# Performance work log

Measured on AMD Instinct MI355X. Metric: run time of the kernel, lower is better.

Reference implementation:

```python
import jax, jax.numpy as jnp
import numpy as np

GROUPS = 32
EPS = 1e-5
NUM_HEADS = 8


def group_norm(x, gamma, beta):
    B, C, H, W = x.shape
    xg = x.reshape(B, GROUPS, C // GROUPS, H, W)
    mean = xg.mean(axis=(2, 3, 4), keepdims=True)
    var = xg.var(axis=(2, 3, 4), keepdims=True)
    xg = (xg - mean) * jax.lax.rsqrt(var + EPS)
    x = xg.reshape(B, C, H, W)
    return x * gamma[None, :, None, None] + beta[None, :, None, None]


def setup_inputs() -> dict:
    key = jax.random.key(0)
    k1, k2, k3 = jax.random.split(key, 3)
    C = 512
    x = jax.random.normal(k1, (16, C, 32, 32), dtype=jnp.float32)
    gn_gamma = jnp.ones((C,), dtype=jnp.float32)
    gn_beta = jnp.zeros((C,), dtype=jnp.float32)
    w_qkv = jax.random.normal(k2, (3 * C, C), dtype=jnp.float32) * 0.02
    b_qkv = jnp.zeros((3 * C,), dtype=jnp.float32)
    w_proj = jax.random.normal(k3, (C, C), dtype=jnp.float32) * 0.02
    b_proj = jnp.zeros((C,), dtype=jnp.float32)
    return {"x": x, "gn_gamma": gn_gamma, "gn_beta": gn_beta,
            "w_qkv": w_qkv, "b_qkv": b_qkv, "w_proj": w_proj, "b_proj": b_proj}


def reference(x, gn_gamma, gn_beta, w_qkv, b_qkv, w_proj, b_proj):
    B, C, H, W = x.shape
    nh = NUM_HEADS
    hd = C // nh
    h = group_norm(x, gn_gamma, gn_beta)
    # 1x1 conv == channel matmul: [B,3C,H,W]
    qkv = jnp.einsum('bchw,oc->bohw', h, w_qkv) + b_qkv[None, :, None, None]
    qkv = qkv.reshape(B, 3, nh, hd, H * W)
    q, k, v = qkv[:, 0], qkv[:, 1], qkv[:, 2]  # [B, nh, hd, HW]
    scale = hd ** -0.5
    # attn[b,n,i,j] = sum_d q[b,n,d,i] * k[b,n,d,j]
    attn = jax.nn.softmax(jnp.einsum('bndi,bndj->bnij', q, k) * scale, axis=-1)
    # h[b,n,d,i] = sum_j v[b,n,d,j] * attn[b,n,i,j]
    h = jnp.einsum('bndj,bnij->bndi', v, attn).reshape(B, C, H, W)
    out = jnp.einsum('bchw,oc->bohw', h, w_proj) + b_proj[None, :, None, None]
    return x + out
```

## Files before the change

### kernel.cpp

```cpp
#include <hip/hip_runtime.h>

typedef __bf16 bf16;
typedef __bf16 bf16x2 __attribute__((ext_vector_type(2)));
typedef __bf16 bf16x4 __attribute__((ext_vector_type(4)));
typedef __bf16 bf16x8 __attribute__((ext_vector_type(8)));
typedef float  f32x4  __attribute__((ext_vector_type(4)));
typedef float  f32x16 __attribute__((ext_vector_type(16)));
typedef unsigned int u32x4 __attribute__((ext_vector_type(4)));

#define MFMA32(a,b,c) __builtin_amdgcn_mfma_f32_32x32x16_bf16((a),(b),(c),0,0,0)

#if __has_builtin(__builtin_amdgcn_exp2f)
#define EXP2(x) __builtin_amdgcn_exp2f(x)
#else
#define EXP2(x) exp2f(x)
#endif

__device__ __forceinline__ void gll16(const void* g, void* l) {
  __builtin_amdgcn_global_load_lds((const __attribute__((address_space(1))) unsigned int*)g,
                                   (__attribute__((address_space(3))) unsigned int*)l, 16, 0, 0);
}

__device__ __forceinline__ unsigned pk2(float a, float b) {
  bf16x2 t = { (bf16)a, (bf16)b };
  return __builtin_bit_cast(unsigned, t);
}

__device__ __forceinline__ void pl32swap(unsigned &x, unsigned &y) {
  asm("v_permlane32_swap_b32 %0, %1" : "+v"(x), "+v"(y));
}

static constexpr int Cc = 512;
static constexpr int Ss = 1024;
#define QSCALE 0.18033688011112042f

__global__ __launch_bounds__(256) void k_wconv(const float* __restrict__ wq, const float* __restrict__ wp,
                                               bf16* __restrict__ wqb, bf16* __restrict__ wpb) {
  const int i = blockIdx.x * 256 + threadIdx.x;
  if (i * 4 < 786432) {
    float4 v = ((const float4*)wq)[i];
    bf16x4 o = { (bf16)v.x, (bf16)v.y, (bf16)v.z, (bf16)v.w };
    ((bf16x4*)wqb)[i] = o;
  } else {
    const int j = i - 786432 / 4;
    float4 v = ((const float4*)wp)[j];
    bf16x4 o = { (bf16)v.x, (bf16)v.y, (bf16)v.z, (bf16)v.w };
    ((bf16x4*)wpb)[j] = o;
  }
}

__global__ __launch_bounds__(256, 2) void k_gnorm(const float* __restrict__ x,
                                                  const float* __restrict__ gamma,
                                                  const float* __restrict__ beta,
                                                  bf16* __restrict__ ht) {
  const int g = blockIdx.x;
  const int b = blockIdx.y;
  const float* base = x + ((size_t)b * Cc + g * 16) * Ss;
  const int tid = threadIdx.x;

  f32x4 xr[16];
  float s = 0.f, sq = 0.f;
  #pragma unroll
  for (int k = 0; k < 16; ++k) {
    xr[k] = ((const f32x4*)base)[k * 256 + tid];
    s  += xr[k][0] + xr[k][1] + xr[k][2] + xr[k][3];
    sq += xr[k][0] * xr[k][0] + xr[k][1] * xr[k][1] + xr[k][2] * xr[k][2] + xr[k][3] * xr[k][3];
  }
  #pragma unroll
  for (int m = 1; m < 64; m <<= 1) { s += __shfl_xor(s, m); sq += __shfl_xor(sq, m); }
  __shared__ float red[8];
  if ((tid & 63) == 0) { red[tid >> 6] = s; red[4 + (tid >> 6)] = sq; }
  __syncthreads();
  const float stot = red[0] + red[1] + red[2] + red[3];
  const float sqt  = red[4] + red[5] + red[6] + red[7];
  const float mean = stot * (1.f / 16384.f);
  const float var  = sqt * (1.f / 16384.f) - mean * mean;
  const float rstd = rsqrtf(var + 1e-5f);

  float ga[16], bb[16];
  #pragma unroll
  for (int k = 0; k < 16; ++k) {
    ga[k] = gamma[g * 16 + k] * rstd;
    bb[k] = beta[g * 16 + k] - mean * ga[k];
  }

  bf16* dst0 = ht + ((size_t)b * Ss + tid * 4) * Cc + g * 16;
  #pragma unroll
  for (int j = 0; j < 4; ++j) {
    bf16x8 o0, o1;
    #pragma unroll
    for (int k = 0; k < 8; ++k)  o0[k] = (bf16)(xr[k][j] * ga[k] + bb[k]);
    #pragma unroll
    for (int k = 0; k < 8; ++k)  o1[k] = (bf16)(xr[8 + k][j] * ga[8 + k] + bb[8 + k]);
    bf16* d = dst0 + (size_t)j * Cc;
    *(bf16x8*)d = o0;
    *(bf16x8*)(d + 8) = o1;
  }
}

template<int MODE>
__global__ __launch_bounds__(256, 2) void k_gemm(const bf16* __restrict__ Aw,
                                                 const bf16* __restrict__ Bt,
                                                 const float* __restrict__ bias,
                                                 bf16* __restrict__ qo, bf16* __restrict__ ko,
                                                 bf16* __restrict__ vo,
                                                 const float* __restrict__ xres,
                                                 float* __restrict__ out) {
  const int nt = blockIdx.x, mt = blockIdx.y, b = blockIdx.z;
  const int M0 = mt * 128, N0 = nt * 128;
  __shared__ __align__(16) char lA[2][16384];
  __shared__ __align__(16) char lB[2][16384];
  const int tid = threadIdx.x;
  const int l = tid & 63, w = tid >> 6;
  const int wm = w >> 1, wn = w & 1;
  const int l31 = l & 31, h = l >> 5;
  const bf16* Bb = Bt + (size_t)b * Ss * Cc;

  const int r8 = tid >> 3, c8 = tid & 7;
  const int csw = (c8 ^ (r8 & 7)) * 16;
  const char* asrc = (const char*)Aw + (size_t)(M0 + r8) * 1024 + csw;
  const char* bsrc = (const char*)Bb + (size_t)(N0 + r8) * 1024 + csw;
  const int dstoff = tid * 16;

  f32x16 acc[2][2];
  #pragma unroll
  for (int i = 0; i < 2; ++i)
    #pragma unroll
    for (int j = 0; j < 2; ++j)
      #pragma unroll
      for (int r = 0; r < 16; ++r) acc[i][j][r] = 0.f;

  const int sw7 = l31 & 7;

  #pragma unroll
  for (int p = 0; p < 4; ++p)
    gll16(asrc + (size_t)p * 32768, (char*)lA[0] + dstoff + p * 4096);
  #pragma unroll
  for (int p = 0; p < 4; ++p)
    gll16(bsrc + (size_t)p * 32768, (char*)lB[0] + dstoff + p * 4096);

  #pragma unroll
  for (int kt = 0; kt < 8; ++kt) {
    const int cur = kt & 1;
    if (kt < 7) {
      #pragma unroll
      for (int p = 0; p < 4; ++p)
        gll16(asrc + (size_t)p * 32768 + (kt + 1) * 128, (char*)lA[cur ^ 1] + dstoff + p * 4096);
      #pragma unroll
      for (int p = 0; p < 4; ++p)
        gll16(bsrc + (size_t)p * 32768 + (kt + 1) * 128, (char*)lB[cur ^ 1] + dstoff + p * 4096);
      asm volatile("s_waitcnt vmcnt(8)" ::: "memory");
    } else {
      asm volatile("s_waitcnt vmcnt(0)" ::: "memory");
    }
    __builtin_amdgcn_s_barrier();
    __builtin_amdgcn_sched_barrier(0);

    __builtin_amdgcn_s_setprio(1);
    #pragma unroll
    for (int kb = 0; kb < 4; ++kb) {
      const int cA0 = ((kb * 2 + h) ^ sw7) * 16;
      const int rA0 = (wm * 2 + 0) * 32 + l31, rA1 = (wm * 2 + 1) * 32 + l31;
      const int rB0 = (wn * 2 + 0) * 32 + l31, rB1 = (wn * 2 + 1) * 32 + l31;
      bf16x8 a0 = *(const bf16x8*)((const char*)lA[cur] + rA0 * 128 + cA0);
      bf16x8 a1 = *(const bf16x8*)((const char*)lA[cur] + rA1 * 128 + cA0);
      bf16x8 b0 = *(const bf16x8*)((const char*)lB[cur] + rB0 * 128 + cA0);
      bf16x8 b1 = *(const bf16x8*)((const char*)lB[cur] + rB1 * 128 + cA0);
      acc[0][0] = MFMA32(a0, b0, acc[0][0]);
      acc[0][1] = MFMA32(a0, b1, acc[0][1]);
      acc[1][0] = MFMA32(a1, b0, acc[1][0]);
      acc[1][1] = MFMA32(a1, b1, acc[1][1]);
    }
    __builtin_amdgcn_s_setprio(0);
    if (kt < 7) {
      asm volatile("s_waitcnt lgkmcnt(0)" ::: "memory");
      __builtin_amdgcn_s_barrier();
    }
  }

  #pragma unroll
  for (int m = 0; m < 2; ++m) {
    const int ofr = M0 + wm * 64 + m * 32;
    #pragma unroll
    for (int n = 0; n < 2; ++n) {
      const int sI = N0 + wn * 64 + n * 32 + l31;
      #pragma unroll
      for (int Qi = 0; Qi < 4; ++Qi) {
        const int rb = Qi * 8 + h * 4;
        float v[4], bi[4];
        #pragma unroll
        for (int r = 0; r < 4; ++r) {
          v[r] = acc[m][n][Qi * 4 + r];
          bi[r] = bias[ofr + rb + r];
        }
        if (MODE == 0) {
          const int which = ofr >> 9;
          const int nh = (ofr >> 6) & 7;
          const int dbase = (ofr & 63) + rb;
          const size_t bh = (size_t)b * 8 + nh;
          if (which == 2) {
            #pragma unroll
            for (int r = 0; r < 4; ++r)
              vo[(bh * 64 + dbase + r) * 1024 + sI] = (bf16)(v[r] + bi[r]);
          } else {
            const float qs = which ? 1.f : QSCALE;
            bf16x4 pk = { (bf16)((v[0] + bi[0]) * qs), (bf16)((v[1] + bi[1]) * qs),
                          (bf16)((v[2] + bi[2]) * qs), (bf16)((v[3] + bi[3]) * qs) };
            bf16* dst = (which ? ko : qo) + (bh * 1024 + sI) * 64 + dbase;
            *(bf16x4*)dst = pk;
          }
        } else {
          #pragma unroll
          for (int r = 0; r < 4; ++r) {
            const size_t idx = ((size_t)b * 512 + ofr + rb + r) * 1024 + sI;
            out[idx] = xres[idx] + bi[r] + v[r];
          }
        }
      }
    }
  }
}

__global__ __launch_bounds__(512, 3) void k_attn(const bf16* __restrict__ qT,
                                                 const bf16* __restrict__ kT,
                                                 const bf16* __restrict__ vv,
                                                 bf16* __restrict__ ao) {
  const int it = blockIdx.x, nh = blockIdx.y, b = blockIdx.z;
  const size_t bh = (size_t)b * 8 + nh;
  const char* kh = (const char*)(kT + bh * 65536);
  const char* vh = (const char*)(vv + bh * 65536);
  __shared__ __align__(16) char smem[32768];
  const int tid = threadIdx.x;
  const int w = tid >> 6, l = tid & 63;
  const int l31 = l & 31, h = l >> 5;

  const int ct = tid >> 6, c3 = ct & 3, c2 = ct >> 2;
  const char* ksrc = kh + (size_t)(c2 * 32 + l31) * 128 + c3 * 32 + h * 16;
  const char* vsrc = vh + (size_t)(c2 * 32 + l31) * 2048 + c3 * 32 + h * 16;
  char* lkdst = smem + tid * 16;
  char* lvdst = smem + 16384 + tid * 16;

  gll16(ksrc, lkdst);
  gll16(vsrc, lvdst);

  const bf16* qrow = qT + bh * 65536 + (size_t)(it * 256 + w * 32 + l31) * 64;
  bf16x8 qf[4];
  #pragma unroll
  for (int kq = 0; kq < 4; ++kq) qf[kq] = *(const bf16x8*)(qrow + kq * 16 + h * 8);

  f32x16 oacc[2];
  #pragma unroll
  for (int dt = 0; dt < 2; ++dt)
    #pragma unroll
    for (int r = 0; r < 16; ++r) oacc[dt][r] = 0.f;
  float lacc0 = 0.f, lacc1 = 0.f;

  int cur = 0;
  for (int t = 0; t < 16; ++t) {
    if (t < 15) {
      gll16(ksrc + (size_t)(t + 1) * 8192, lkdst + (cur ^ 1) * 8192);
      gll16(vsrc + (size_t)(t + 1) * 128,  lvdst + (cur ^ 1) * 8192);
      asm volatile("s_waitcnt vmcnt(2)" ::: "memory");
    } else {
      asm volatile("s_waitcnt vmcnt(0)" ::: "memory");
    }
    __builtin_amdgcn_s_barrier();
    __builtin_amdgcn_sched_barrier(0);

    const char* lkc = smem + cur * 8192;
    const char* lvc = smem + 16384 + cur * 8192;

    f32x16 sf[2];
    #pragma unroll
    for (int r = 0; r < 16; ++r) { sf[0][r] = 0.f; sf[1][r] = 0.f; }
    __builtin_amdgcn_s_setprio(1);
    #pragma unroll
    for (int kq = 0; kq < 4; ++kq) {
      bf16x8 a0 = *(const bf16x8*)(lkc + kq * 1024 + l * 16);
      bf16x8 a1 = *(const bf16x8*)(lkc + (4 + kq) * 1024 + l * 16);
      sf[0] = MFMA32(a0, qf[kq], sf[0]);
      sf[1] = MFMA32(a1, qf[kq], sf[1]);
    }
    __builtin_amdgcn_s_setprio(0);

    unsigned pw[2][4][2];
    #pragma unroll
    for (int jt = 0; jt < 2; ++jt) {
      #pragma unroll
      for (int Qi = 0; Qi < 4; ++Qi) {
        const float p0 = EXP2(sf[jt][Qi * 4 + 0]);
        const float p1 = EXP2(sf[jt][Qi * 4 + 1]);
        const float p2 = EXP2(sf[jt][Qi * 4 + 2]);
        const float p3 = EXP2(sf[jt][Qi * 4 + 3]);
        lacc0 += p0 + p1; lacc1 += p2 + p3;
        pw[jt][Qi][0] = pk2(p0, p1);
        pw[jt][Qi][1] = pk2(p2, p3);
      }
    }

    bf16x8 pb[4];
    #pragma unroll
    for (int s = 0; s < 4; ++s) {
      const int jt = s >> 1, sq = s & 1;
      unsigned x0 = pw[jt][2 * sq][0], y0 = pw[jt][2 * sq + 1][0];
      unsigned x1 = pw[jt][2 * sq][1], y1 = pw[jt][2 * sq + 1][1];
      pl32swap(x0, y0);
      pl32swap(x1, y1);
      u32x4 wv = { x0, x1, y0, y1 };
      pb[s] = __builtin_bit_cast(bf16x8, wv);
    }

    __builtin_amdgcn_s_setprio(1);
    #pragma unroll
    for (int dt = 0; dt < 2; ++dt) {
      #pragma unroll
      for (int s = 0; s < 4; ++s) {
        bf16x8 av = *(const bf16x8*)(lvc + (dt * 4 + s) * 1024 + l * 16);
        oacc[dt] = MFMA32(av, pb[s], oacc[dt]);
      }
    }
    __builtin_amdgcn_s_setprio(0);
    if (t < 15) {
      asm volatile("s_waitcnt lgkmcnt(0)" ::: "memory");
      __builtin_amdgcn_s_barrier();
    }
    cur ^= 1;
  }

  float ls = lacc0 + lacc1;
  ls += __shfl_xor(ls, 32);
  const float rinv = 1.f / ls;

  bf16* aor = ao + ((size_t)b * 1024 + it * 256 + w * 32 + l31) * 512 + nh * 64;
  #pragma unroll
  for (int dt = 0; dt < 2; ++dt) {
    #pragma unroll
    for (int Qi = 0; Qi < 4; ++Qi) {
      bf16x4 o = { (bf16)(oacc[dt][Qi * 4 + 0] * rinv), (bf16)(oacc[dt][Qi * 4 + 1] * rinv),
                   (bf16)(oacc[dt][Qi * 4 + 2] * rinv), (bf16)(oacc[dt][Qi * 4 + 3] * rinv) };
      *(bf16x4*)(aor + dt * 32 + Qi * 8 + h * 4) = o;
    }
  }
}

extern "C" void kernel_launch(void* const* d_in, const int* in_sizes, int n_in,
                              void* d_out, int out_size, void* d_ws, size_t ws_size,
                              hipStream_t stream) {
  (void)in_sizes; (void)n_in; (void)out_size; (void)ws_size;
  const float* x   = (const float*)d_in[0];
  const float* gam = (const float*)d_in[1];
  const float* bet = (const float*)d_in[2];
  const float* wq  = (const float*)d_in[3];
  const float* bq  = (const float*)d_in[4];
  const float* wp  = (const float*)d_in[5];
  const float* bp  = (const float*)d_in[6];
  float* out = (float*)d_out;

  bf16* ws  = (bf16*)d_ws;
  bf16* ht  = ws;
  bf16* qT  = ws + 8388608;
  bf16* kT  = ws + 16777216;
  bf16* vv  = ws + 25165824;
  bf16* wqb = ws + 33554432;
  bf16* wpb = ws + 34340864;

  k_wconv<<<1024, 256, 0, stream>>>(wq, wp, wqb, wpb);
  k_gnorm<<<dim3(32, 16), 256, 0, stream>>>(x, gam, bet, ht);
  k_gemm<0><<<dim3(8, 12, 16), 256, 0, stream>>>(wqb, ht, bq, qT, kT, vv, nullptr, nullptr);
  k_attn<<<dim3(4, 8, 16), 512, 0, stream>>>(qT, kT, vv, ht);
  k_gemm<1><<<dim3(8, 4, 16), 256, 0, stream>>>(wpb, ht, bp, nullptr, nullptr, nullptr, x, out);
}
```

Measured before the change: 125.8 us.

## Process two query blocks per warp in attention to reuse K/V LDS fragments

Each warp in the attention kernel now handles 64 query rows (two 32-row blocks) instead of 32. Every K and V fragment read from LDS feeds two MFMAs, and the grid is halved to 256 blocks. This halves the number of LDS reads and global K/V tile loads per query. In exchange it doubles the accumulators and Q registers, lowers the occupancy bound from 3 to 2 blocks per CU, and leaves fewer blocks to fill the GPU.

```diff
diff --git a/kernel.cpp b/kernel.cpp
--- a/kernel.cpp
+++ b/kernel.cpp
@@ -221,7 +221,7 @@
   }
 }
 
-__global__ __launch_bounds__(512, 3) void k_attn(const bf16* __restrict__ qT,
+__global__ __launch_bounds__(512, 2) void k_attn(const bf16* __restrict__ qT,
                                                  const bf16* __restrict__ kT,
                                                  const bf16* __restrict__ vv,
                                                  bf16* __restrict__ ao) {
@@ -234,6 +234,14 @@
   const int w = tid >> 6, l = tid & 63;
   const int l31 = l & 31, h = l >> 5;
 
+  const bf16* qrow = qT + bh * 65536 + (size_t)(it * 512 + w * 64 + l31) * 64;
+  bf16x8 qf[2][4];
+  #pragma unroll
+  for (int qb = 0; qb < 2; ++qb)
+    #pragma unroll
+    for (int kq = 0; kq < 4; ++kq)
+      qf[qb][kq] = *(const bf16x8*)(qrow + qb * 2048 + kq * 16 + h * 8);
+
   const int ct = tid >> 6, c3 = ct & 3, c2 = ct >> 2;
   const char* ksrc = kh + (size_t)(c2 * 32 + l31) * 128 + c3 * 32 + h * 16;
   const char* vsrc = vh + (size_t)(c2 * 32 + l31) * 2048 + c3 * 32 + h * 16;
@@ -243,17 +251,14 @@
   gll16(ksrc, lkdst);
   gll16(vsrc, lvdst);
 
-  const bf16* qrow = qT + bh * 65536 + (size_t)(it * 256 + w * 32 + l31) * 64;
-  bf16x8 qf[4];
-  #pragma unroll
-  for (int kq = 0; kq < 4; ++kq) qf[kq] = *(const bf16x8*)(qrow + kq * 16 + h * 8);
-
-  f32x16 oacc[2];
-  #pragma unroll
-  for (int dt = 0; dt < 2; ++dt)
-    #pragma unroll
-    for (int r = 0; r < 16; ++r) oacc[dt][r] = 0.f;
-  float lacc0 = 0.f, lacc1 = 0.f;
+  f32x16 oacc[2][2];
+  #pragma unroll
+  for (int qb = 0; qb < 2; ++qb)
+    #pragma unroll
+    for (int dt = 0; dt < 2; ++dt)
+      #pragma unroll
+      for (int r = 0; r < 16; ++r) oacc[qb][dt][r] = 0.f;
+  float lacc[2][2] = {{0.f, 0.f}, {0.f, 0.f}};
 
   int cur = 0;
   for (int t = 0; t < 16; ++t) {
@@ -270,44 +275,43 @@
     const char* lkc = smem + cur * 8192;
     const char* lvc = smem + 16384 + cur * 8192;
 
-    f32x16 sf[2];
-    #pragma unroll
-    for (int r = 0; r < 16; ++r) { sf[0][r] = 0.f; sf[1][r] = 0.f; }
-    __builtin_amdgcn_s_setprio(1);
-    #pragma unroll
-    for (int kq = 0; kq < 4; ++kq) {
-      bf16x8 a0 = *(const bf16x8*)(lkc + kq * 1024 + l * 16);
-      bf16x8 a1 = *(const bf16x8*)(lkc + (4 + kq) * 1024 + l * 16);
-      sf[0] = MFMA32(a0, qf[kq], sf[0]);
-      sf[1] = MFMA32(a1, qf[kq], sf[1]);
-    }
-    __builtin_amdgcn_s_setprio(0);
-
-    unsigned pw[2][4][2];
+    bf16x8 pb[2][4];
     #pragma unroll
     for (int jt = 0; jt < 2; ++jt) {
-      #pragma unroll
-      for (int Qi = 0; Qi < 4; ++Qi) {
-        const float p0 = EXP2(sf[jt][Qi * 4 + 0]);
-        const float p1 = EXP2(sf[jt][Qi * 4 + 1]);
-        const float p2 = EXP2(sf[jt][Qi * 4 + 2]);
-        const float p3 = EXP2(sf[jt][Qi * 4 + 3]);
-        lacc0 += p0 + p1; lacc1 += p2 + p3;
-        pw[jt][Qi][0] = pk2(p0, p1);
-        pw[jt][Qi][1] = pk2(p2, p3);
-      }
-    }
-
-    bf16x8 pb[4];
-    #pragma unroll
-    for (int s = 0; s < 4; ++s) {
-      const int jt = s >> 1, sq = s & 1;
-      unsigned x0 = pw[jt][2 * sq][0], y0 = pw[jt][2 * sq + 1][0];
-      unsigned x1 = pw[jt][2 * sq][1], y1 = pw[jt][2 * sq + 1][1];
-      pl32swap(x0, y0);
-      pl32swap(x1, y1);
-      u32x4 wv = { x0, x1, y0, y1 };
-      pb[s] = __builtin_bit_cast(bf16x8, wv);
+      f32x16 sf[2];
+      #pragma unroll
+      for (int r = 0; r < 16; ++r) { sf[0][r] = 0.f; sf[1][r] = 0.f; }
+      __builtin_amdgcn_s_setprio(1);
+      #pragma unroll
+      for (int kq = 0; kq < 4; ++kq) {
+        bf16x8 a = *(const bf16x8*)(lkc + (jt * 4 + kq) * 1024 + l * 16);
+        sf[0] = MFMA32(a, qf[0][kq], sf[0]);
+        sf[1] = MFMA32(a, qf[1][kq], sf[1]);
+      }
+      __builtin_amdgcn_s_setprio(0);
+      #pragma unroll
+      for (int qb = 0; qb < 2; ++qb) {
+        unsigned pw[4][2];
+        #pragma unroll
+        for (int Qi = 0; Qi < 4; ++Qi) {
+          const float p0 = EXP2(sf[qb][Qi * 4 + 0]);
+          const float p1 = EXP2(sf[qb][Qi * 4 + 1]);
+          const float p2 = EXP2(sf[qb][Qi * 4 + 2]);
+          const float p3 = EXP2(sf[qb][Qi * 4 + 3]);
+          lacc[qb][0] += p0 + p1; lacc[qb][1] += p2 + p3;
+          pw[Qi][0] = pk2(p0, p1);
+          pw[Qi][1] = pk2(p2, p3);
+        }
+        #pragma unroll
+        for (int sq = 0; sq < 2; ++sq) {
+          unsigned x0 = pw[2 * sq][0], y0 = pw[2 * sq + 1][0];
+          unsigned x1 = pw[2 * sq][1], y1 = pw[2 * sq + 1][1];
+          pl32swap(x0, y0);
+          pl32swap(x1, y1);
+          u32x4 wv = { x0, x1, y0, y1 };
+          pb[qb][jt * 2 + sq] = __builtin_bit_cast(bf16x8, wv);
+        }
+      }
     }
 
     __builtin_amdgcn_s_setprio(1);
@@ -316,7 +320,8 @@
       #pragma unroll
       for (int s = 0; s < 4; ++s) {
         bf16x8 av = *(const bf16x8*)(lvc + (dt * 4 + s) * 1024 + l * 16);
-        oacc[dt] = MFMA32(av, pb[s], oacc[dt]);
+        oacc[0][dt] = MFMA32(av, pb[0][s], oacc[0][dt]);
+        oacc[1][dt] = MFMA32(av, pb[1][s], oacc[1][dt]);
       }
     }
     __builtin_amdgcn_s_setprio(0);
@@ -327,18 +332,20 @@
     cur ^= 1;
   }
 
-  float ls = lacc0 + lacc1;
-  ls += __shfl_xor(ls, 32);
-  const float rinv = 1.f / ls;
-
-  bf16* aor = ao + ((size_t)b * 1024 + it * 256 + w * 32 + l31) * 512 + nh * 64;
-  #pragma unroll
-  for (int dt = 0; dt < 2; ++dt) {
-    #pragma unroll
-    for (int Qi = 0; Qi < 4; ++Qi) {
-      bf16x4 o = { (bf16)(oacc[dt][Qi * 4 + 0] * rinv), (bf16)(oacc[dt][Qi * 4 + 1] * rinv),
-                   (bf16)(oacc[dt][Qi * 4 + 2] * rinv), (bf16)(oacc[dt][Qi * 4 + 3] * rinv) };
-      *(bf16x4*)(aor + dt * 32 + Qi * 8 + h * 4) = o;
+  #pragma unroll
+  for (int qb = 0; qb < 2; ++qb) {
+    float ls = lacc[qb][0] + lacc[qb][1];
+    ls += __shfl_xor(ls, 32);
+    const float rinv = 1.f / ls;
+    bf16* aor = ao + ((size_t)b * 1024 + it * 512 + w * 64 + qb * 32 + l31) * 512 + nh * 64;
+    #pragma unroll
+    for (int dt = 0; dt < 2; ++dt) {
+      #pragma unroll
+      for (int Qi = 0; Qi < 4; ++Qi) {
+        bf16x4 o = { (bf16)(oacc[qb][dt][Qi * 4 + 0] * rinv), (bf16)(oacc[qb][dt][Qi * 4 + 1] * rinv),
+                     (bf16)(oacc[qb][dt][Qi * 4 + 2] * rinv), (bf16)(oacc[qb][dt][Qi * 4 + 3] * rinv) };
+        *(bf16x4*)(aor + dt * 32 + Qi * 8 + h * 4) = o;
+      }
     }
   }
 }
@@ -367,6 +374,6 @@
   k_wconv<<<1024, 256, 0, stream>>>(wq, wp, wqb, wpb);
   k_gnorm<<<dim3(32, 16), 256, 0, stream>>>(x, gam, bet, ht);
   k_gemm<0><<<dim3(8, 12, 16), 256, 0, stream>>>(wqb, ht, bq, qT, kT, vv, nullptr, nullptr);
-  k_attn<<<dim3(4, 8, 16), 512, 0, stream>>>(qT, kT, vv, ht);
+  k_attn<<<dim3(2, 8, 16), 512, 0, stream>>>(qT, kT, vv, ht);
   k_gemm<1><<<dim3(8, 4, 16), 256, 0, stream>>>(wpb, ht, bp, nullptr, nullptr, nullptr, x, out);
 }
```

After: 126.1 us. Within noise of the previous version (+0.2%).
